# Performance work log

Hardware: AMD Instinct MI355X
Metric: run time of the kernel (lower is better)

The kernel has to match this reference:

```python
import jax, jax.numpy as jnp
import numpy as np

B, SX, SC, D, H = 4, 2048, 2048, 512, 8
DK = D // H


def setup_inputs() -> dict:
    key = jax.random.key(0)
    ks = jax.random.split(key, 12)
    s = 0.02
    return {
        "x": jax.random.normal(ks[0], (B, SX, D), jnp.float32),
        "c": jax.random.normal(ks[1], (B, SC, D), jnp.float32),
        "Wq": jax.random.normal(ks[2], (D, D), jnp.float32) * s,
        "bq": jnp.zeros((D,), jnp.float32),
        "Wk": jax.random.normal(ks[3], (D, D), jnp.float32) * s,
        "bk": jnp.zeros((D,), jnp.float32),
        "Wv": jax.random.normal(ks[4], (D, D), jnp.float32) * s,
        "bv": jnp.zeros((D,), jnp.float32),
        "Wo": jax.random.normal(ks[5], (D, D), jnp.float32) * s,
        "bo": jnp.zeros((D,), jnp.float32),
        "rel_table": jax.random.normal(ks[6], (SX + SC - 1, H), jnp.float32) * s,
    }


def reference(x, c, Wq, bq, Wk, bk, Wv, bv, Wo, bo, rel_table):
    b = x.shape[0]
    # projections (torch Linear: y = x @ W.T + b)
    q = (x @ Wq.T + bq).reshape(b, SX, H, DK).transpose(0, 2, 1, 3)  # (B,H,Sx,dk)
    k = (c @ Wk.T + bk).reshape(b, SC, H, DK).transpose(0, 2, 1, 3)  # (B,H,Sc,dk)
    v = (c @ Wv.T + bv).reshape(b, SC, H, DK).transpose(0, 2, 1, 3)
    scale = 1.0 / jnp.sqrt(jnp.float32(DK))
    scores = jnp.einsum('bhqd,bhkd->bhqk', q, k) * scale  # (B,H,Sx,Sc)
    # relative position bias: index (Sx,Sc) into table (Sx+Sc-1, H)
    rel_idx = jnp.arange(SX)[:, None] - jnp.arange(SC)[None, :] + (SC - 1)
    bias = rel_table[rel_idx].transpose(2, 0, 1)  # (H,Sx,Sc)
    scores = scores + bias[None]
    # causal_mask=False -> False * -1e9 adds 0 (no-op); omitted
    weights = jax.nn.softmax(scores, axis=-1)
    out = jnp.einsum('bhqk,bhkd->bhqd', weights, v)  # (B,H,Sx,dk)
    out = out.transpose(0, 2, 1, 3).reshape(b, SX, D)
    return out @ Wo.T + bo
```

## Files before the change

### kernel.cpp

```cpp
#include <hip/hip_runtime.h>
#include <hip/hip_bf16.h>
#include <cstdint>
#include <cstddef>

typedef __bf16 bf16;
typedef __bf16 bf16x4 __attribute__((ext_vector_type(4)));
typedef __bf16 bf16x8 __attribute__((ext_vector_type(8)));
typedef float f32x4 __attribute__((ext_vector_type(4)));
typedef float f32x16 __attribute__((ext_vector_type(16)));

#define MFMA16(a, b, c) __builtin_amdgcn_mfma_f32_16x16x32_bf16((a), (b), (c), 0, 0, 0)
#define MFMA32(a, b, c) __builtin_amdgcn_mfma_f32_32x32x16_bf16((a), (b), (c), 0, 0, 0)
#define GLD16(g, l) __builtin_amdgcn_global_load_lds( \
    (const __attribute__((address_space(1))) void*)(g), \
    (__attribute__((address_space(3))) void*)(l), 16, 0, 0)

constexpr int Bsz = 4, SX = 2048, SC = 2048, Dm = 512, H = 8, DK = 64;
constexpr float L2E = 1.4426950408889634f;

__global__ __launch_bounds__(256) void cvt_all(
    const float* __restrict__ x, const float* __restrict__ c,
    const float* __restrict__ Wq, const float* __restrict__ Wk,
    const float* __restrict__ Wv, const float* __restrict__ Wo,
    const float* __restrict__ rel,
    bf16* __restrict__ xcOut, bf16* __restrict__ wOut, float* __restrict__ relT)
{
    int blk = blockIdx.x;
    if (blk < 4096) {
        int i = (blk * 256 + threadIdx.x) * 8;
        const float* src = (i < 4194304) ? x : c;
        int off = i & 4194303;
        float4 v0 = *(const float4*)(src + off);
        float4 v1 = *(const float4*)(src + off + 4);
        bf16x8 o = { (bf16)v0.x, (bf16)v0.y, (bf16)v0.z, (bf16)v0.w,
                     (bf16)v1.x, (bf16)v1.y, (bf16)v1.z, (bf16)v1.w };
        *(bf16x8*)(xcOut + i) = o;
    } else if (blk < 4608) {
        int i = ((blk - 4096) * 256 + threadIdx.x) * 8;
        int w = i >> 18;
        int off = i & 262143;
        const float* src = (w == 0) ? Wq : (w == 1) ? Wk : (w == 2) ? Wv : Wo;
        float4 v0 = *(const float4*)(src + off);
        float4 v1 = *(const float4*)(src + off + 4);
        bf16x8 o = { (bf16)v0.x, (bf16)v0.y, (bf16)v0.z, (bf16)v0.w,
                     (bf16)v1.x, (bf16)v1.y, (bf16)v1.z, (bf16)v1.w };
        *(bf16x8*)(wOut + i) = o;
    } else {
        int q = blk - 4608;
        int h = q >> 4;
        int i = (q & 15) * 256 + threadIdx.x;
        if (i < SX + SC - 1) relT[h * (SX + SC - 1) + i] = rel[i * H + h] * L2E;
    }
}

__global__ __launch_bounds__(256, 3) void qkv_gemm(
    const bf16* __restrict__ Xbf, const bf16* __restrict__ Cbf,
    const bf16* __restrict__ Wbf,
    const float* __restrict__ bq, const float* __restrict__ bk,
    const float* __restrict__ bv,
    bf16* __restrict__ Qw, bf16* __restrict__ Kw, bf16* __restrict__ Vw)
{
    __shared__ alignas(16) bf16 As[128 * 64];
    __shared__ alignas(16) bf16 Bs[128 * 64];

    const int proj = blockIdx.x >> 2;
    const int n0 = (blockIdx.x & 3) * 128;
    const int m0 = blockIdx.y * 128;
    const bf16* A = (proj == 0) ? Xbf : Cbf;
    const bf16* W = Wbf + proj * 262144;
    const float* bias = (proj == 0) ? bq : (proj == 1) ? bk : bv;

    const int t = threadIdx.x;
    const int wid = t >> 6, lane = t & 63, lr = lane & 15, lq = lane >> 4;
    const int wm = (wid & 1) * 64, wn = (wid >> 1) * 64;

    const int rl = lane >> 3;
    const int ch = (lane & 7) ^ rl;

    f32x4 acc[4][4];
#pragma unroll
    for (int i = 0; i < 4; i++)
#pragma unroll
        for (int j = 0; j < 4; j++) acc[i][j] = f32x4{0.f, 0.f, 0.f, 0.f};

    for (int k0 = 0; k0 < Dm; k0 += 64) {
        const bf16* ga = A + (size_t)(m0 + wid * 32 + rl) * Dm + k0 + ch * 8;
        const bf16* gb = W + (size_t)(n0 + wid * 32 + rl) * Dm + k0 + ch * 8;
#pragma unroll
        for (int g = 0; g < 4; g++)
            GLD16(ga + (size_t)g * 8 * Dm, &As[(wid * 32 + g * 8) * 64]);
#pragma unroll
        for (int g = 0; g < 4; g++)
            GLD16(gb + (size_t)g * 8 * Dm, &Bs[(wid * 32 + g * 8) * 64]);
        __syncthreads();
#pragma unroll
        for (int ks = 0; ks < 2; ks++) {
            bf16x8 af[4], bfr[4];
#pragma unroll
            for (int mt = 0; mt < 4; mt++)
                af[mt] = *(const bf16x8*)&As[(wm + mt * 16 + lr) * 64 + (((ks * 4 + lq) ^ (lr & 7)) * 8)];
#pragma unroll
            for (int nt = 0; nt < 4; nt++)
                bfr[nt] = *(const bf16x8*)&Bs[(wn + nt * 16 + lr) * 64 + (((ks * 4 + lq) ^ (lr & 7)) * 8)];
#pragma unroll
            for (int mt = 0; mt < 4; mt++)
#pragma unroll
                for (int nt = 0; nt < 4; nt++)
                    acc[mt][nt] = MFMA16(af[mt], bfr[nt], acc[mt][nt]);
        }
        __syncthreads();
    }

#pragma unroll
    for (int mt = 0; mt < 4; mt++) {
#pragma unroll
        for (int nt = 0; nt < 4; nt++) {
#pragma unroll
            for (int r = 0; r < 4; r++) {
                int m = m0 + wm + mt * 16 + lq * 4 + r;
                int n = n0 + wn + nt * 16 + lr;
                float v = acc[mt][nt][r] + bias[n];
                int bh = (m >> 11) * 8 + (n >> 6);
                int key = m & 2047, dk = n & 63;
                if (proj == 0) {
                    Qw[(size_t)(bh * 2048 + key) * 64 + dk] = (bf16)v;
                } else if (proj == 1) {
                    int idx = ((((bh * 64 + (key >> 5)) * 4 + (dk >> 4)) * 2 + ((dk >> 3) & 1)) * 32
                               + (key & 31)) * 8 + (dk & 7);
                    Kw[idx] = (bf16)v;
                } else {
                    int idx = (((((bh * 32 + (key >> 6)) * 4 + ((key >> 4) & 3)) * 2 + (dk >> 5)) * 2
                                + ((key >> 3) & 1)) * 32 + (dk & 31)) * 8 + (key & 7);
                    Vw[idx] = (bf16)v;
                }
            }
        }
    }
}

__global__ __launch_bounds__(256, 2) void out_gemm(
    const bf16* __restrict__ A, const bf16* __restrict__ W,
    const float* __restrict__ bias, float* __restrict__ Y)
{
    __shared__ alignas(16) bf16 As[64 * 64];
    __shared__ alignas(16) bf16 Bs[128 * 64];

    const int t = threadIdx.x;
    const int n0 = blockIdx.x * 128;
    const int m0 = blockIdx.y * 64;
    const int wid = t >> 6, lane = t & 63, lr = lane & 15, lq = lane >> 4;
    const int wn = wid * 32;

    const int rl = lane >> 3;
    const int ch = (lane & 7) ^ rl;

    f32x4 acc[4][2];
#pragma unroll
    for (int i = 0; i < 4; i++)
#pragma unroll
        for (int j = 0; j < 2; j++) acc[i][j] = f32x4{0.f, 0.f, 0.f, 0.f};

    for (int k0 = 0; k0 < Dm; k0 += 64) {
        const bf16* ga = A + (size_t)(m0 + wid * 16 + rl) * Dm + k0 + ch * 8;
        const bf16* gb = W + (size_t)(n0 + wid * 32 + rl) * Dm + k0 + ch * 8;
#pragma unroll
        for (int g = 0; g < 2; g++)
            GLD16(ga + (size_t)g * 8 * Dm, &As[(wid * 16 + g * 8) * 64]);
#pragma unroll
        for (int g = 0; g < 4; g++)
            GLD16(gb + (size_t)g * 8 * Dm, &Bs[(wid * 32 + g * 8) * 64]);
        __syncthreads();
#pragma unroll
        for (int ks = 0; ks < 2; ks++) {
            bf16x8 af[4], bfr[2];
#pragma unroll
            for (int mt = 0; mt < 4; mt++)
                af[mt] = *(const bf16x8*)&As[(mt * 16 + lr) * 64 + (((ks * 4 + lq) ^ (lr & 7)) * 8)];
#pragma unroll
            for (int nt = 0; nt < 2; nt++)
                bfr[nt] = *(const bf16x8*)&Bs[(wn + nt * 16 + lr) * 64 + (((ks * 4 + lq) ^ (lr & 7)) * 8)];
#pragma unroll
            for (int mt = 0; mt < 4; mt++)
#pragma unroll
                for (int nt = 0; nt < 2; nt++)
                    acc[mt][nt] = MFMA16(af[mt], bfr[nt], acc[mt][nt]);
        }
        __syncthreads();
    }

#pragma unroll
    for (int mt = 0; mt < 4; mt++) {
#pragma unroll
        for (int nt = 0; nt < 2; nt++) {
#pragma unroll
            for (int r = 0; r < 4; r++) {
                int m = m0 + mt * 16 + lq * 4 + r;
                int n = n0 + wn + nt * 16 + lr;
                Y[(size_t)m * Dm + n] = acc[mt][nt][r] + bias[n];
            }
        }
    }
}

constexpr int PST = 72;

__global__ __launch_bounds__(128, 4) void attn_kernel(
    const bf16* __restrict__ Qm, const bf16* __restrict__ Kf,
    const bf16* __restrict__ Vf, const float* __restrict__ relT,
    bf16* __restrict__ Oa)
{
    const int id = blockIdx.x;
    const int xcd = id & 7, j = id >> 3;
    const int bh = xcd + 8 * (j & 3);
    const int q0 = (j >> 2) * 32;
    const int h = bh & 7, b = bh >> 3;
    const int t = threadIdx.x;
    const int wid = t >> 6, lane = t & 63;
    const int l31 = lane & 31, l5 = lane >> 5;

    __shared__ alignas(16) char sm[19456];
    bf16*  Ps   = (bf16*)(sm + wid * 4608);
    float* Osum = (float*)(sm + 9216);
    float* Bsl  = (float*)(sm + 18432) + wid * 96;
    float* Ls1  = (float*)(sm + 19200);
    float* Lfin = (float*)(sm + 19328);

    const bf16* Qb = Qm + (size_t)bh * SC * DK;
    const bf16* Kb = Kf + (size_t)bh * 64 * 2048;
    const bf16* Vb = Vf + (size_t)bh * 32 * 4096;
    const float* rT = relT + h * (SX + SC - 1);

    bf16x8 qf[4];
#pragma unroll
    for (int ks = 0; ks < 4; ks++)
        qf[ks] = *(const bf16x8*)&Qb[(size_t)(q0 + l31) * DK + ks * 16 + l5 * 8];

    f32x16 oacc[2];
#pragma unroll
    for (int ng = 0; ng < 2; ng++)
#pragma unroll
        for (int r = 0; r < 16; r++) oacc[ng][r] = 0.f;
    float lsum = 0.f;

    const float sc = 0.125f * L2E;
    const int kw0 = wid << 10;

#pragma unroll 2
    for (int tt = 0; tt < 16; ++tt) {
        const int k0 = kw0 + tt * 64;
        int i0 = q0 - k0 + 1984;
        Bsl[lane] = rT[i0 + lane];
        if (lane < 31) Bsl[64 + lane] = rT[i0 + 64 + lane];

#pragma unroll
        for (int kg = 0; kg < 2; kg++) {
            const bf16* kb = Kb + (size_t)((k0 >> 5) + kg) * 2048 + lane * 8;
            f32x16 s;
#pragma unroll
            for (int r = 0; r < 16; r++) s[r] = 0.f;
#pragma unroll
            for (int ks = 0; ks < 4; ks++) {
                bf16x8 kf = *(const bf16x8*)(kb + ks * 512);
                s = MFMA32(kf, qf[ks], s);
            }
#pragma unroll
            for (int r4 = 0; r4 < 4; r4++) {
                float p[4];
#pragma unroll
                for (int r0 = 0; r0 < 4; r0++) {
                    int n = r0 + 8 * r4 + 4 * l5;
                    int ib = 63 + l31 - (kg * 32 + n);
                    p[r0] = __builtin_amdgcn_exp2f(s[r4 * 4 + r0] * sc + Bsl[ib]);
                    lsum += p[r0];
                }
                bf16x4 pk = { (bf16)p[0], (bf16)p[1], (bf16)p[2], (bf16)p[3] };
                *(bf16x4*)&Ps[l31 * PST + kg * 32 + 8 * r4 + 4 * l5] = pk;
            }
        }
        bf16x8 pf[4];
#pragma unroll
        for (int ks = 0; ks < 4; ks++)
            pf[ks] = *(const bf16x8*)&Ps[l31 * PST + ks * 16 + l5 * 8];
        const bf16* vb = Vb + (size_t)(k0 >> 6) * 4096 + lane * 8;
#pragma unroll
        for (int ng = 0; ng < 2; ng++) {
#pragma unroll
            for (int ks = 0; ks < 4; ks++) {
                bf16x8 vf = *(const bf16x8*)(vb + ng * 512 + ks * 1024);
                oacc[ng] = MFMA32(pf[ks], vf, oacc[ng]);
            }
        }
    }

    lsum += __shfl_xor(lsum, 32, 64);
    if (wid == 1) {
        if (lane < 32) Ls1[l31] = lsum;
        float* Op = Osum + lane * 36;
#pragma unroll
        for (int ng = 0; ng < 2; ng++)
#pragma unroll
            for (int q = 0; q < 4; q++) {
                f32x4 v = { oacc[ng][q * 4 + 0], oacc[ng][q * 4 + 1],
                            oacc[ng][q * 4 + 2], oacc[ng][q * 4 + 3] };
                *(f32x4*)(Op + ng * 16 + q * 4) = v;
            }
    }
    __syncthreads();
    if (wid == 0) {
        lsum += Ls1[l31];
        const float* Op = Osum + lane * 36;
#pragma unroll
        for (int ng = 0; ng < 2; ng++)
#pragma unroll
            for (int q = 0; q < 4; q++) {
                f32x4 v = *(const f32x4*)(Op + ng * 16 + q * 4);
#pragma unroll
                for (int r0 = 0; r0 < 4; r0++) oacc[ng][q * 4 + r0] += v[r0];
            }
        if (lane < 32) Lfin[l31] = lsum;
#pragma unroll
        for (int r4 = 0; r4 < 4; r4++) {
            float4 lv = *(const float4*)&Lfin[8 * r4 + 4 * l5];
            float rv[4] = { 1.f / lv.x, 1.f / lv.y, 1.f / lv.z, 1.f / lv.w };
#pragma unroll
            for (int ng = 0; ng < 2; ng++) {
#pragma unroll
                for (int r0 = 0; r0 < 4; r0++) {
                    int row = r0 + 8 * r4 + 4 * l5;
                    Oa[((size_t)(b * SX + q0 + row)) * Dm + h * 64 + ng * 32 + l31] =
                        (bf16)(oacc[ng][r4 * 4 + r0] * rv[r0]);
                }
            }
        }
    }
}

extern "C" void kernel_launch(void* const* d_in, const int* in_sizes, int n_in,
                              void* d_out, int out_size, void* d_ws, size_t ws_size,
                              hipStream_t stream)
{
    (void)in_sizes; (void)n_in; (void)out_size; (void)ws_size;

    const float* x   = (const float*)d_in[0];
    const float* c   = (const float*)d_in[1];
    const float* Wq  = (const float*)d_in[2];
    const float* bq  = (const float*)d_in[3];
    const float* Wk  = (const float*)d_in[4];
    const float* bk  = (const float*)d_in[5];
    const float* Wv  = (const float*)d_in[6];
    const float* bv  = (const float*)d_in[7];
    const float* Wo  = (const float*)d_in[8];
    const float* bo  = (const float*)d_in[9];
    const float* rel = (const float*)d_in[10];

    char* ws = (char*)d_ws;
    bf16*  Wbf  = (bf16*)ws;
    bf16*  Xbf  = (bf16*)(ws + (2u << 20));
    bf16*  Cbf  = Xbf + 4194304;
    bf16*  Aw   = (bf16*)(ws + (2u << 20));
    bf16*  Qw   = (bf16*)(ws + (18u << 20));
    bf16*  Kw   = (bf16*)(ws + (26u << 20));
    bf16*  Vw   = (bf16*)(ws + (34u << 20));
    float* relT = (float*)(ws + (42u << 20));

    cvt_all<<<4736, 256, 0, stream>>>(x, c, Wq, Wk, Wv, Wo, rel, Xbf, Wbf, relT);

    qkv_gemm<<<dim3(12, 64), 256, 0, stream>>>(Xbf, Cbf, Wbf, bq, bk, bv, Qw, Kw, Vw);

    attn_kernel<<<2048, 128, 0, stream>>>(Qw, Kw, Vw, relT, Aw);

    out_gemm<<<dim3(4, 128), 256, 0, stream>>>(Aw, Wbf + 3 * 262144, bo, (float*)d_out);
}
```

Measured before the change: 205.2 us.

## Double-buffer LDS tiles in projection GEMMs and prefetch V early in attention

Both projection GEMMs now use two LDS buffers, issuing the next K-tile's async global-to-LDS loads before computing on the current tile. This removes one barrier per iteration and overlaps memory latency with MFMA work. The attention loop issues its V fragment loads at the top of each iteration so they overlap the QK^T and softmax work, and its unroll drops from 2 to 1. In exchange, LDS per block doubles, so qkv_gemm's launch bound falls from 3 to 2 blocks per CU, and attention needs more VGPRs to hold the prefetched V.

```diff
diff --git a/kernel.cpp b/kernel.cpp
--- a/kernel.cpp
+++ b/kernel.cpp
@@ -53,15 +53,15 @@
     }
 }
 
-__global__ __launch_bounds__(256, 3) void qkv_gemm(
+__global__ __launch_bounds__(256, 2) void qkv_gemm(
     const bf16* __restrict__ Xbf, const bf16* __restrict__ Cbf,
     const bf16* __restrict__ Wbf,
     const float* __restrict__ bq, const float* __restrict__ bk,
     const float* __restrict__ bv,
     bf16* __restrict__ Qw, bf16* __restrict__ Kw, bf16* __restrict__ Vw)
 {
-    __shared__ alignas(16) bf16 As[128 * 64];
-    __shared__ alignas(16) bf16 Bs[128 * 64];
+    __shared__ alignas(16) bf16 As[2][128 * 64];
+    __shared__ alignas(16) bf16 Bs[2][128 * 64];
 
     const int proj = blockIdx.x >> 2;
     const int n0 = (blockIdx.x & 3) * 128;
@@ -77,38 +77,48 @@
     const int rl = lane >> 3;
     const int ch = (lane & 7) ^ rl;
 
+    const bf16* ga0 = A + (size_t)(m0 + wid * 32 + rl) * Dm + ch * 8;
+    const bf16* gb0 = W + (size_t)(n0 + wid * 32 + rl) * Dm + ch * 8;
+
     f32x4 acc[4][4];
 #pragma unroll
     for (int i = 0; i < 4; i++)
 #pragma unroll
         for (int j = 0; j < 4; j++) acc[i][j] = f32x4{0.f, 0.f, 0.f, 0.f};
 
-    for (int k0 = 0; k0 < Dm; k0 += 64) {
-        const bf16* ga = A + (size_t)(m0 + wid * 32 + rl) * Dm + k0 + ch * 8;
-        const bf16* gb = W + (size_t)(n0 + wid * 32 + rl) * Dm + k0 + ch * 8;
-#pragma unroll
-        for (int g = 0; g < 4; g++)
-            GLD16(ga + (size_t)g * 8 * Dm, &As[(wid * 32 + g * 8) * 64]);
-#pragma unroll
-        for (int g = 0; g < 4; g++)
-            GLD16(gb + (size_t)g * 8 * Dm, &Bs[(wid * 32 + g * 8) * 64]);
+#pragma unroll
+    for (int g = 0; g < 4; g++) {
+        GLD16(ga0 + (size_t)g * 8 * Dm, &As[0][(wid * 32 + g * 8) * 64]);
+        GLD16(gb0 + (size_t)g * 8 * Dm, &Bs[0][(wid * 32 + g * 8) * 64]);
+    }
+
+    for (int k = 0; k < 8; k++) {
         __syncthreads();
+        const int cur = k & 1;
+        if (k < 7) {
+            const bf16* ga = ga0 + (k + 1) * 64;
+            const bf16* gb = gb0 + (k + 1) * 64;
+#pragma unroll
+            for (int g = 0; g < 4; g++) {
+                GLD16(ga + (size_t)g * 8 * Dm, &As[cur ^ 1][(wid * 32 + g * 8) * 64]);
+                GLD16(gb + (size_t)g * 8 * Dm, &Bs[cur ^ 1][(wid * 32 + g * 8) * 64]);
+            }
+        }
 #pragma unroll
         for (int ks = 0; ks < 2; ks++) {
             bf16x8 af[4], bfr[4];
 #pragma unroll
             for (int mt = 0; mt < 4; mt++)
-                af[mt] = *(const bf16x8*)&As[(wm + mt * 16 + lr) * 64 + (((ks * 4 + lq) ^ (lr & 7)) * 8)];
+                af[mt] = *(const bf16x8*)&As[cur][(wm + mt * 16 + lr) * 64 + (((ks * 4 + lq) ^ (lr & 7)) * 8)];
 #pragma unroll
             for (int nt = 0; nt < 4; nt++)
-                bfr[nt] = *(const bf16x8*)&Bs[(wn + nt * 16 + lr) * 64 + (((ks * 4 + lq) ^ (lr & 7)) * 8)];
+                bfr[nt] = *(const bf16x8*)&Bs[cur][(wn + nt * 16 + lr) * 64 + (((ks * 4 + lq) ^ (lr & 7)) * 8)];
 #pragma unroll
             for (int mt = 0; mt < 4; mt++)
 #pragma unroll
                 for (int nt = 0; nt < 4; nt++)
                     acc[mt][nt] = MFMA16(af[mt], bfr[nt], acc[mt][nt]);
         }
-        __syncthreads();
     }
 
 #pragma unroll
@@ -142,8 +152,8 @@
     const bf16* __restrict__ A, const bf16* __restrict__ W,
     const float* __restrict__ bias, float* __restrict__ Y)
 {
-    __shared__ alignas(16) bf16 As[64 * 64];
-    __shared__ alignas(16) bf16 Bs[128 * 64];
+    __shared__ alignas(16) bf16 As[2][64 * 64];
+    __shared__ alignas(16) bf16 Bs[2][128 * 64];
 
     const int t = threadIdx.x;
     const int n0 = blockIdx.x * 128;
@@ -154,38 +164,50 @@
     const int rl = lane >> 3;
     const int ch = (lane & 7) ^ rl;
 
+    const bf16* ga0 = A + (size_t)(m0 + wid * 16 + rl) * Dm + ch * 8;
+    const bf16* gb0 = W + (size_t)(n0 + wid * 32 + rl) * Dm + ch * 8;
+
     f32x4 acc[4][2];
 #pragma unroll
     for (int i = 0; i < 4; i++)
 #pragma unroll
         for (int j = 0; j < 2; j++) acc[i][j] = f32x4{0.f, 0.f, 0.f, 0.f};
 
-    for (int k0 = 0; k0 < Dm; k0 += 64) {
-        const bf16* ga = A + (size_t)(m0 + wid * 16 + rl) * Dm + k0 + ch * 8;
-        const bf16* gb = W + (size_t)(n0 + wid * 32 + rl) * Dm + k0 + ch * 8;
-#pragma unroll
-        for (int g = 0; g < 2; g++)
-            GLD16(ga + (size_t)g * 8 * Dm, &As[(wid * 16 + g * 8) * 64]);
-#pragma unroll
-        for (int g = 0; g < 4; g++)
-            GLD16(gb + (size_t)g * 8 * Dm, &Bs[(wid * 32 + g * 8) * 64]);
+#pragma unroll
+    for (int g = 0; g < 2; g++)
+        GLD16(ga0 + (size_t)g * 8 * Dm, &As[0][(wid * 16 + g * 8) * 64]);
+#pragma unroll
+    for (int g = 0; g < 4; g++)
+        GLD16(gb0 + (size_t)g * 8 * Dm, &Bs[0][(wid * 32 + g * 8) * 64]);
+
+    for (int k = 0; k < 8; k++) {
         __syncthreads();
+        const int cur = k & 1;
+        if (k < 7) {
+            const bf16* ga = ga0 + (k + 1) * 64;
+            const bf16* gb = gb0 + (k + 1) * 64;
+#pragma unroll
+            for (int g = 0; g < 2; g++)
+                GLD16(ga + (size_t)g * 8 * Dm, &As[cur ^ 1][(wid * 16 + g * 8) * 64]);
+#pragma unroll
+            for (int g = 0; g < 4; g++)
+                GLD16(gb + (size_t)g * 8 * Dm, &Bs[cur ^ 1][(wid * 32 + g * 8) * 64]);
+        }
 #pragma unroll
         for (int ks = 0; ks < 2; ks++) {
             bf16x8 af[4], bfr[2];
 #pragma unroll
             for (int mt = 0; mt < 4; mt++)
-                af[mt] = *(const bf16x8*)&As[(mt * 16 + lr) * 64 + (((ks * 4 + lq) ^ (lr & 7)) * 8)];
+                af[mt] = *(const bf16x8*)&As[cur][(mt * 16 + lr) * 64 + (((ks * 4 + lq) ^ (lr & 7)) * 8)];
 #pragma unroll
             for (int nt = 0; nt < 2; nt++)
-                bfr[nt] = *(const bf16x8*)&Bs[(wn + nt * 16 + lr) * 64 + (((ks * 4 + lq) ^ (lr & 7)) * 8)];
+                bfr[nt] = *(const bf16x8*)&Bs[cur][(wn + nt * 16 + lr) * 64 + (((ks * 4 + lq) ^ (lr & 7)) * 8)];
 #pragma unroll
             for (int mt = 0; mt < 4; mt++)
 #pragma unroll
                 for (int nt = 0; nt < 2; nt++)
                     acc[mt][nt] = MFMA16(af[mt], bfr[nt], acc[mt][nt]);
         }
-        __syncthreads();
     }
 
 #pragma unroll
@@ -245,12 +267,20 @@
     const float sc = 0.125f * L2E;
     const int kw0 = wid << 10;
 
-#pragma unroll 2
+#pragma unroll 1
     for (int tt = 0; tt < 16; ++tt) {
         const int k0 = kw0 + tt * 64;
         int i0 = q0 - k0 + 1984;
         Bsl[lane] = rT[i0 + lane];
         if (lane < 31) Bsl[64 + lane] = rT[i0 + 64 + lane];
+
+        const bf16* vb = Vb + (size_t)(k0 >> 6) * 4096 + lane * 8;
+        bf16x8 vf[8];
+#pragma unroll
+        for (int ng = 0; ng < 2; ng++)
+#pragma unroll
+            for (int ks = 0; ks < 4; ks++)
+                vf[ng * 4 + ks] = *(const bf16x8*)(vb + ng * 512 + ks * 1024);
 
 #pragma unroll
         for (int kg = 0; kg < 2; kg++) {
@@ -281,15 +311,11 @@
 #pragma unroll
         for (int ks = 0; ks < 4; ks++)
             pf[ks] = *(const bf16x8*)&Ps[l31 * PST + ks * 16 + l5 * 8];
-        const bf16* vb = Vb + (size_t)(k0 >> 6) * 4096 + lane * 8;
-#pragma unroll
-        for (int ng = 0; ng < 2; ng++) {
-#pragma unroll
-            for (int ks = 0; ks < 4; ks++) {
-                bf16x8 vf = *(const bf16x8*)(vb + ng * 512 + ks * 1024);
-                oacc[ng] = MFMA32(pf[ks], vf, oacc[ng]);
-            }
-        }
+#pragma unroll
+        for (int ng = 0; ng < 2; ng++)
+#pragma unroll
+            for (int ks = 0; ks < 4; ks++)
+                oacc[ng] = MFMA32(pf[ks], vf[ng * 4 + ks], oacc[ng]);
     }
 
     lsum += __shfl_xor(lsum, 32, 64);
```

Result: slower. 214.6 us (+4.6%).

## Stage GEMM epilogues through LDS and read relative bias directly from global

Applied to the files above, without the earlier changes.

The QKV projection epilogue now writes results into shared memory in the final Q/K/V layouts and then copies whole 16-byte vectors to global memory, replacing scattered 2-byte stores. The output GEMM likewise stages fp32 results in LDS and writes coalesced float4 rows. The attention kernel drops its per-tile LDS staging of the relative-bias slice and instead loads four consecutive bias values per lane with an unaligned vector load from global or L2, also reducing the main loop unroll to 1. This adds an extra LDS round trip and barrier per GEMM block, and the attention change relies on cache hits for the overlapping bias reads.

```diff
diff --git a/kernel.cpp b/kernel.cpp
--- a/kernel.cpp
+++ b/kernel.cpp
@@ -7,6 +7,7 @@
 typedef __bf16 bf16x4 __attribute__((ext_vector_type(4)));
 typedef __bf16 bf16x8 __attribute__((ext_vector_type(8)));
 typedef float f32x4 __attribute__((ext_vector_type(4)));
+typedef float f32x4u __attribute__((ext_vector_type(4), aligned(4)));
 typedef float f32x16 __attribute__((ext_vector_type(16)));
 
 #define MFMA16(a, b, c) __builtin_amdgcn_mfma_f32_16x16x32_bf16((a), (b), (c), 0, 0, 0)
@@ -60,8 +61,9 @@
     const float* __restrict__ bv,
     bf16* __restrict__ Qw, bf16* __restrict__ Kw, bf16* __restrict__ Vw)
 {
-    __shared__ alignas(16) bf16 As[128 * 64];
-    __shared__ alignas(16) bf16 Bs[128 * 64];
+    __shared__ alignas(16) bf16 smem[16384];
+    bf16* As = smem;
+    bf16* Bs = smem + 8192;
 
     const int proj = blockIdx.x >> 2;
     const int n0 = (blockIdx.x & 3) * 128;
@@ -111,29 +113,46 @@
         __syncthreads();
     }
 
+    bf16* Es = smem;
 #pragma unroll
     for (int mt = 0; mt < 4; mt++) {
 #pragma unroll
         for (int nt = 0; nt < 4; nt++) {
+            int nl = wn + nt * 16 + lr;
+            int head = nl >> 6, dk = nl & 63;
+            float bv_ = bias[n0 + nl];
 #pragma unroll
             for (int r = 0; r < 4; r++) {
-                int m = m0 + wm + mt * 16 + lq * 4 + r;
-                int n = n0 + wn + nt * 16 + lr;
-                float v = acc[mt][nt][r] + bias[n];
-                int bh = (m >> 11) * 8 + (n >> 6);
-                int key = m & 2047, dk = n & 63;
-                if (proj == 0) {
-                    Qw[(size_t)(bh * 2048 + key) * 64 + dk] = (bf16)v;
-                } else if (proj == 1) {
-                    int idx = ((((bh * 64 + (key >> 5)) * 4 + (dk >> 4)) * 2 + ((dk >> 3) & 1)) * 32
-                               + (key & 31)) * 8 + (dk & 7);
-                    Kw[idx] = (bf16)v;
-                } else {
-                    int idx = (((((bh * 32 + (key >> 6)) * 4 + ((key >> 4) & 3)) * 2 + (dk >> 5)) * 2
-                                + ((key >> 3) & 1)) * 32 + (dk & 31)) * 8 + (key & 7);
-                    Vw[idx] = (bf16)v;
-                }
-            }
+                int keyl = wm + mt * 16 + lq * 4 + r;
+                float v = acc[mt][nt][r] + bv_;
+                int off;
+                if (proj == 0)
+                    off = keyl * 64 + dk;
+                else if (proj == 1)
+                    off = ((((keyl >> 5) * 4 + (dk >> 4)) * 2 + ((dk >> 3) & 1)) * 32
+                           + (keyl & 31)) * 8 + (dk & 7);
+                else
+                    off = (((((keyl >> 6) * 4 + ((keyl >> 4) & 3)) * 2 + (dk >> 5)) * 2
+                            + ((keyl >> 3) & 1)) * 32 + (dk & 31)) * 8 + (keyl & 7);
+                Es[head * 8192 + off] = (bf16)v;
+            }
+        }
+    }
+    __syncthreads();
+
+    const int b = m0 >> 11, key0 = m0 & 2047;
+#pragma unroll
+    for (int hh = 0; hh < 2; hh++) {
+        int bh = b * 8 + (n0 >> 6) + hh;
+        size_t base;
+        bf16* dst;
+        if (proj == 0)      { base = (size_t)(bh * 2048 + key0) * 64;        dst = Qw; }
+        else if (proj == 1) { base = (size_t)(bh * 64 + (key0 >> 5)) * 2048; dst = Kw; }
+        else                { base = (size_t)(bh * 32 + (key0 >> 6)) * 4096; dst = Vw; }
+#pragma unroll
+        for (int i = 0; i < 4; i++) {
+            int e = (i * 256 + t) * 8;
+            *(bf16x8*)(dst + base + e) = *(const bf16x8*)&Es[hh * 8192 + e];
         }
     }
 }
@@ -142,8 +161,10 @@
     const bf16* __restrict__ A, const bf16* __restrict__ W,
     const float* __restrict__ bias, float* __restrict__ Y)
 {
-    __shared__ alignas(16) bf16 As[64 * 64];
-    __shared__ alignas(16) bf16 Bs[128 * 64];
+    __shared__ alignas(16) char osm[32768];
+    bf16* As = (bf16*)osm;
+    bf16* Bs = (bf16*)(osm + 8192);
+    float* Es = (float*)osm;
 
     const int t = threadIdx.x;
     const int n0 = blockIdx.x * 128;
@@ -192,13 +213,21 @@
     for (int mt = 0; mt < 4; mt++) {
 #pragma unroll
         for (int nt = 0; nt < 2; nt++) {
+            int nl = wn + nt * 16 + lr;
+            float bv_ = bias[n0 + nl];
 #pragma unroll
             for (int r = 0; r < 4; r++) {
-                int m = m0 + mt * 16 + lq * 4 + r;
-                int n = n0 + wn + nt * 16 + lr;
-                Y[(size_t)m * Dm + n] = acc[mt][nt][r] + bias[n];
-            }
-        }
+                int ml = mt * 16 + lq * 4 + r;
+                Es[ml * 128 + nl] = acc[mt][nt][r] + bv_;
+            }
+        }
+    }
+    __syncthreads();
+#pragma unroll
+    for (int i = 0; i < 8; i++) {
+        int e = i * 256 + t;
+        int row = e >> 5, c4 = (e & 31) * 4;
+        *(f32x4*)(Y + (size_t)(m0 + row) * Dm + n0 + c4) = *(const f32x4*)&Es[row * 128 + c4];
     }
 }
 
@@ -218,12 +247,11 @@
     const int wid = t >> 6, lane = t & 63;
     const int l31 = lane & 31, l5 = lane >> 5;
 
-    __shared__ alignas(16) char sm[19456];
+    __shared__ alignas(16) char sm[18688];
     bf16*  Ps   = (bf16*)(sm + wid * 4608);
     float* Osum = (float*)(sm + 9216);
-    float* Bsl  = (float*)(sm + 18432) + wid * 96;
-    float* Ls1  = (float*)(sm + 19200);
-    float* Lfin = (float*)(sm + 19328);
+    float* Ls1  = (float*)(sm + 18432);
+    float* Lfin = (float*)(sm + 18560);
 
     const bf16* Qb = Qm + (size_t)bh * SC * DK;
     const bf16* Kb = Kf + (size_t)bh * 64 * 2048;
@@ -245,12 +273,10 @@
     const float sc = 0.125f * L2E;
     const int kw0 = wid << 10;
 
-#pragma unroll 2
+#pragma unroll 1
     for (int tt = 0; tt < 16; ++tt) {
         const int k0 = kw0 + tt * 64;
-        int i0 = q0 - k0 + 1984;
-        Bsl[lane] = rT[i0 + lane];
-        if (lane < 31) Bsl[64 + lane] = rT[i0 + 64 + lane];
+        const int i0 = q0 - k0 + 1984;
 
 #pragma unroll
         for (int kg = 0; kg < 2; kg++) {
@@ -265,12 +291,12 @@
             }
 #pragma unroll
             for (int r4 = 0; r4 < 4; r4++) {
+                int Cb = i0 + 60 + l31 - kg * 32 - 8 * r4 - 4 * l5;
+                f32x4u B4 = *(const f32x4u*)(rT + Cb);
                 float p[4];
 #pragma unroll
                 for (int r0 = 0; r0 < 4; r0++) {
-                    int n = r0 + 8 * r4 + 4 * l5;
-                    int ib = 63 + l31 - (kg * 32 + n);
-                    p[r0] = __builtin_amdgcn_exp2f(s[r4 * 4 + r0] * sc + Bsl[ib]);
+                    p[r0] = __builtin_amdgcn_exp2f(s[r4 * 4 + r0] * sc + B4[3 - r0]);
                     lsum += p[r0];
                 }
                 bf16x4 pk = { (bf16)p[0], (bf16)p[1], (bf16)p[2], (bf16)p[3] };
```

Result: faster. 189.8 us (-7.5%).
